# Performance work log

Measured on AMD Instinct MI355X. Metric: run time of the kernel, lower is better.

Reference implementation:

```python
import jax, jax.numpy as jnp
import numpy as np
import math

EPS = 1e-5

def layernorm(x, g, b):
    mu = jnp.mean(x, axis=-1, keepdims=True)
    var = jnp.var(x, axis=-1, keepdims=True)
    return (x - mu) * jax.lax.rsqrt(var + EPS) * g + b

def setup_inputs() -> dict:
    key = jax.random.key(0)
    ks = jax.random.split(key, 12)
    B, T, E, H = 4, 2048, 128, 8
    D = H * E          # 1024
    F = 4 * D          # 4096
    s = 0.02
    return {
        "X":     jax.random.normal(ks[0], (B, T, E), jnp.float32),
        "ln1_g": jnp.ones((E,), jnp.float32),
        "ln1_b": jnp.zeros((E,), jnp.float32),
        "Wq":    jax.random.normal(ks[1], (H, E, E), jnp.float32) * s,
        "bq":    jax.random.normal(ks[2], (H, E), jnp.float32) * s,
        "Wk":    jax.random.normal(ks[3], (H, E, E), jnp.float32) * s,
        "bk":    jax.random.normal(ks[4], (H, E), jnp.float32) * s,
        "Wv":    jax.random.normal(ks[5], (H, E, E), jnp.float32) * s,
        "bv":    jax.random.normal(ks[6], (H, E), jnp.float32) * s,
        "ln2_g": jnp.ones((D,), jnp.float32),
        "ln2_b": jnp.zeros((D,), jnp.float32),
        "W1":    jax.random.normal(ks[7], (D, F), jnp.float32) * s,
        "b1":    jax.random.normal(ks[8], (F,), jnp.float32) * s,
        "W2":    jax.random.normal(ks[9], (F, E), jnp.float32) * s,
        "b2":    jax.random.normal(ks[10], (E,), jnp.float32) * s,
    }

def reference(X, ln1_g, ln1_b, Wq, bq, Wk, bk, Wv, bv, ln2_g, ln2_b, W1, b1, W2, b2):
    B, T, E = X.shape
    Xn = layernorm(X, ln1_g, ln1_b)                       # [B,T,E]
    # per-head projections, vectorized over heads
    q = jnp.einsum('bte,hef->bhtf', Xn, Wq) + bq[None, :, None, :]
    k = jnp.einsum('bte,hef->bhtf', Xn, Wk) + bk[None, :, None, :]
    v = jnp.einsum('bte,hef->bhtf', Xn, Wv) + bv[None, :, None, :]
    scores = jnp.einsum('bhtf,bhsf->bhts', q, k) / math.sqrt(E)
    # causal mask: positions with s > t set to -inf (triu offset=1)
    t_idx = jnp.arange(T)
    mask = t_idx[None, :] > t_idx[:, None]                # [T,S], True above diag
    scores = jnp.where(mask[None, None], -jnp.inf, scores)
    # NOTE: original code softmaxes over dim = ndim-2, i.e. the QUERY axis
    attn = jax.nn.softmax(scores, axis=-2)
    out = jnp.einsum('bhts,bhsf->bhtf', attn, v)          # [B,H,T,E]
    # concat heads along last dim (head order preserved)
    concat = jnp.transpose(out, (0, 2, 1, 3)).reshape(B, T, -1)  # [B,T,H*E]
    h = layernorm(concat, ln2_g, ln2_b)
    mid = jax.nn.gelu(h @ W1 + b1, approximate=False)
    return mid @ W2 + b2                                   # [B,T,E]
```

## Files before the change

### kernel.cpp

```cpp
#include <hip/hip_runtime.h>
#include <hip/hip_bf16.h>
#include <math.h>

typedef __hip_bfloat16 bf16;
typedef __attribute__((ext_vector_type(8))) short short8;
typedef __attribute__((ext_vector_type(4))) float floatx4;

#define B_ 4
#define T_ 2048
#define E_ 128
#define H_ 8
#define D_ 1024
#define F_ 4096
#define M_ 8192

static __device__ __forceinline__ float b2f(bf16 v){ return __bfloat162float(v); }
static __device__ __forceinline__ bf16  f2b(float v){ return __float2bfloat16(v); }
static __device__ __forceinline__ short f2bs(float v){ bf16 h = __float2bfloat16(v); return *(short*)&h; }

static __device__ __forceinline__ void glds16(const bf16* g, void* l){
  __builtin_amdgcn_global_load_lds((const __attribute__((address_space(1))) void*)g,
                                   (__attribute__((address_space(3))) void*)l, 16, 0, 0);
}

__global__ void detect_dtype_k(const unsigned int* __restrict__ g, int* __restrict__ flag){
  if (threadIdx.x == 0) flag[0] = (g[0] == 0x3F803F80u) ? 1 : 0;
}

__global__ void convert_misc_k(const void* s0, const void* s1, const void* s2, const void* s3,
                               const void* s4, const void* s5, const void* s6, const void* s7,
                               const void* s8,
                               bf16* g1, bf16* b1, bf16* bqkv, bf16* g2, bf16* b2l,
                               bf16* bb1, bf16* bb2, const int* __restrict__ flag){
  int i = blockIdx.x * 256 + threadIdx.x;
  if (i >= 9600) return;
  int fl = flag[0];
  const void* src; bf16* dst; int off;
  if      (i <  128){ src = s0; dst = g1;          off = i;        }
  else if (i <  256){ src = s1; dst = b1;          off = i - 128;  }
  else if (i < 1280){ src = s2; dst = bqkv;        off = i - 256;  }
  else if (i < 2304){ src = s3; dst = bqkv + 1024; off = i - 1280; }
  else if (i < 3328){ src = s4; dst = bqkv + 2048; off = i - 2304; }
  else if (i < 4352){ src = s5; dst = g2;          off = i - 3328; }
  else if (i < 5376){ src = s6; dst = b2l;         off = i - 4352; }
  else if (i < 9472){ src = s7; dst = bb1;         off = i - 5376; }
  else              { src = s8; dst = bb2;         off = i - 9472; }
  dst[off] = fl ? ((const bf16*)src)[off] : f2b(((const float*)src)[off]);
}

__global__ __launch_bounds__(256) void transpose_cvt_k(const void* __restrict__ src, bf16* __restrict__ dst,
                                                       int R, int C, const int* __restrict__ flag){
  __shared__ float tile[32][33];
  int r0 = blockIdx.y * 32, c0 = blockIdx.x * 32;
  int tx = threadIdx.x & 31, ty = threadIdx.x >> 5;
  int fl = flag[0];
  #pragma unroll
  for (int i = 0; i < 32; i += 8){
    size_t idx = (size_t)(r0 + ty + i) * C + c0 + tx;
    tile[ty + i][tx] = fl ? b2f(((const bf16*)src)[idx]) : ((const float*)src)[idx];
  }
  __syncthreads();
  #pragma unroll
  for (int i = 0; i < 32; i += 8){
    dst[(size_t)(c0 + ty + i) * R + r0 + tx] = f2b(tile[tx][ty + i]);
  }
}

__global__ __launch_bounds__(256) void transpose_qkv_k(const void* __restrict__ Wq, const void* __restrict__ Wk,
                                                       const void* __restrict__ Wv, bf16* __restrict__ dst,
                                                       const int* __restrict__ flag){
  __shared__ float tile[32][33];
  int sel = blockIdx.z >> 3, h = blockIdx.z & 7;
  const void* src = (sel == 0) ? Wq : (sel == 1) ? Wk : Wv;
  size_t mo = (size_t)h * E_ * E_;
  bf16* d = dst + (size_t)sel * H_ * E_ * E_ + mo;
  int r0 = blockIdx.y * 32, c0 = blockIdx.x * 32;
  int tx = threadIdx.x & 31, ty = threadIdx.x >> 5;
  int fl = flag[0];
  #pragma unroll
  for (int i = 0; i < 32; i += 8){
    size_t idx = mo + (size_t)(r0 + ty + i) * E_ + c0 + tx;
    tile[ty + i][tx] = fl ? b2f(((const bf16*)src)[idx]) : ((const float*)src)[idx];
  }
  __syncthreads();
  #pragma unroll
  for (int i = 0; i < 32; i += 8){
    d[(size_t)(c0 + ty + i) * E_ + r0 + tx] = f2b(tile[tx][ty + i]);
  }
}

__global__ __launch_bounds__(256) void ln1_k(const void* __restrict__ X, const bf16* __restrict__ g,
                                             const bf16* __restrict__ b, bf16* __restrict__ out,
                                             const int* __restrict__ flag){
  int row = blockIdx.x * 4 + (threadIdx.x >> 6);
  int lane = threadIdx.x & 63;
  float x0, x1;
  if (flag[0]){
    const bf16* xp = (const bf16*)X + (size_t)row * E_;
    x0 = b2f(xp[lane]); x1 = b2f(xp[lane + 64]);
  } else {
    const float* xp = (const float*)X + (size_t)row * E_;
    x0 = xp[lane]; x1 = xp[lane + 64];
  }
  float s  = x0 + x1;
  float s2 = x0 * x0 + x1 * x1;
  #pragma unroll
  for (int o = 32; o > 0; o >>= 1){ s += __shfl_xor(s, o, 64); s2 += __shfl_xor(s2, o, 64); }
  float mu  = s * (1.0f / 128.0f);
  float var = s2 * (1.0f / 128.0f) - mu * mu;
  float rs  = rsqrtf(var + 1e-5f);
  out[(size_t)row * E_ + lane]      = f2b((x0 - mu) * rs * b2f(g[lane])      + b2f(b[lane]));
  out[(size_t)row * E_ + lane + 64] = f2b((x1 - mu) * rs * b2f(g[lane + 64]) + b2f(b[lane + 64]));
}

template<int EPI>
__global__ __launch_bounds__(256, 3) void gemm_mfma_k(
    const bf16* __restrict__ A, const bf16* __restrict__ Bt,
    const bf16* __restrict__ bias, void* __restrict__ out,
    int K, const int* __restrict__ flag)
{
  __shared__ __align__(16) short As[2][4][128][8];
  __shared__ __align__(16) short Bs[2][4][128][8];
  int tid = threadIdx.x;
  int lane = tid & 63, w = tid >> 6;
  int quad = lane >> 4, l16 = lane & 15;
  int wm = w & 1, wn = w >> 1;
  int m0 = blockIdx.y * 128;
  int n0, nit;
  size_t kstart;
  if (EPI == 3){ n0 = 0; int kc = K >> 3; kstart = (size_t)blockIdx.x * kc; nit = kc >> 5; }
  else         { n0 = blockIdx.x * 128; kstart = 0; nit = K >> 5; }

  int seg0 = w * 2, seg1 = w * 2 + 1;
  int kq0 = seg0 & 3, mb0 = (seg0 >> 2) * 64;
  int kq1 = seg1 & 3, mb1 = (seg1 >> 2) * 64;
  const bf16* pa0 = A  + (size_t)(m0 + mb0 + lane) * K + kstart + kq0 * 8;
  const bf16* pa1 = A  + (size_t)(m0 + mb1 + lane) * K + kstart + kq1 * 8;
  const bf16* pb0 = Bt + (size_t)(n0 + mb0 + lane) * K + kstart + kq0 * 8;
  const bf16* pb1 = Bt + (size_t)(n0 + mb1 + lane) * K + kstart + kq1 * 8;
  uint4 ra0 = *(const uint4*)pa0, ra1 = *(const uint4*)pa1;
  uint4 rb0 = *(const uint4*)pb0, rb1 = *(const uint4*)pb1;

  floatx4 acc[4][4];
  #pragma unroll
  for (int i = 0; i < 4; i++)
    #pragma unroll
    for (int j = 0; j < 4; j++) acc[i][j] = (floatx4){0.f, 0.f, 0.f, 0.f};

  for (int it = 0; it < nit; it++){
    int buf = it & 1;
    *(uint4*)&As[buf][kq0][mb0 + lane][0] = ra0;
    *(uint4*)&As[buf][kq1][mb1 + lane][0] = ra1;
    *(uint4*)&Bs[buf][kq0][mb0 + lane][0] = rb0;
    *(uint4*)&Bs[buf][kq1][mb1 + lane][0] = rb1;
    __syncthreads();
    if (it + 1 < nit){
      int ko = (it + 1) << 5;
      ra0 = *(const uint4*)(pa0 + ko); ra1 = *(const uint4*)(pa1 + ko);
      rb0 = *(const uint4*)(pb0 + ko); rb1 = *(const uint4*)(pb1 + ko);
    }
    short8 af[4], bfr[4];
    #pragma unroll
    for (int i = 0; i < 4; i++) af[i]  = *(const short8*)&As[buf][quad][wm * 64 + i * 16 + l16][0];
    #pragma unroll
    for (int j = 0; j < 4; j++) bfr[j] = *(const short8*)&Bs[buf][quad][wn * 64 + j * 16 + l16][0];
    #pragma unroll
    for (int i = 0; i < 4; i++)
      #pragma unroll
      for (int j = 0; j < 4; j++)
        acc[i][j] = __builtin_amdgcn_mfma_f32_16x16x32_bf16(af[i], bfr[j], acc[i][j], 0, 0, 0);
  }

  bf16* po = (EPI == 3) ? (bf16*)out + (size_t)blockIdx.x * M_ * E_ : nullptr;
  #pragma unroll
  for (int i = 0; i < 4; i++){
    #pragma unroll
    for (int j = 0; j < 4; j++){
      int nn = n0 + wn * 64 + j * 16 + l16;
      float bv = (EPI == 3) ? 0.0f : b2f(bias[nn]);
      if (EPI == 0){
        int sel = nn >> 10, h = (nn >> 7) & 7, f = nn & 127;
        size_t SZ = (size_t)B_ * H_ * T_ * E_;
        int mmb = m0 + wm * 64 + i * 16 + quad * 4;
        int b = mmb >> 11, t = mmb & (T_ - 1);
        if (sel < 2){
          #pragma unroll
          for (int r = 0; r < 4; r++)
            ((bf16*)out)[(size_t)sel * SZ + (((size_t)(b * H_ + h) * T_ + t + r) * E_) + f] =
              f2b(acc[i][j][r] + bv);
        } else {
          ushort4 pk;
          #pragma unroll
          for (int r = 0; r < 4; r++) ((short*)&pk)[r] = f2bs(acc[i][j][r] + bv);
          *(ushort4*)((bf16*)out + 2 * SZ + (((size_t)(b * H_ + h) * E_ + f) * T_) + t) = pk;
        }
      } else {
        #pragma unroll
        for (int r = 0; r < 4; r++){
          int mm = m0 + wm * 64 + i * 16 + quad * 4 + r;
          po[(size_t)mm * E_ + nn] = f2b(acc[i][j][r] + bv);
        }
      }
    }
  }
}

__global__ __launch_bounds__(512, 2) void mlp1_swz_k(
    const bf16* __restrict__ A, const bf16* __restrict__ Bt,
    const bf16* __restrict__ bias, bf16* __restrict__ out)
{
  __shared__ __align__(16) short As[4][256][32];
  __shared__ __align__(16) short Bs[4][256][32];
  constexpr int K  = D_;
  constexpr int NK = K / 32;
  constexpr int BUFB = 256 * 32 * 2;

  int tid = threadIdx.x;
  int lane = tid & 63, w = tid >> 6;
  int quad = lane >> 4, l16 = lane & 15;
  int wm = w & 1, wn = w >> 1;
  int orig = blockIdx.y * 16 + blockIdx.x;
  int swz = (orig & 7) * 64 + (orig >> 3);
  int m0 = (swz >> 4) * 256, n0 = (swz & 15) * 256;

  int u0 = w * 2, u1 = u0 + 1;
  int rl = lane >> 2;
  int cg = (lane & 3) ^ ((lane >> 3) & 3);
  const bf16* gA0 = A  + (size_t)(m0 + u0 * 16 + rl) * K + cg * 8;
  const bf16* gA1 = A  + (size_t)(m0 + u1 * 16 + rl) * K + cg * 8;
  const bf16* gB0 = Bt + (size_t)(n0 + u0 * 16 + rl) * K + cg * 8;
  const bf16* gB1 = Bt + (size_t)(n0 + u1 * 16 + rl) * K + cg * 8;

  int offA[2][4], offB[4];
  #pragma unroll
  for (int h = 0; h < 2; h++)
    #pragma unroll
    for (int i = 0; i < 4; i++){
      int ra = wm * 128 + h * 64 + i * 16 + l16;
      offA[h][i] = (ra << 6) + ((quad ^ ((ra >> 1) & 3)) << 4);
    }
  #pragma unroll
  for (int j = 0; j < 4; j++){
    int rb = wn * 64 + j * 16 + l16;
    offB[j] = (rb << 6) + ((quad ^ ((rb >> 1) & 3)) << 4);
  }

  #pragma unroll
  for (int t = 0; t < 3; t++){
    int ko = t * 32;
    glds16(gA0 + ko, &As[t][u0 * 16][0]);
    glds16(gA1 + ko, &As[t][u1 * 16][0]);
    glds16(gB0 + ko, &Bs[t][u0 * 16][0]);
    glds16(gB1 + ko, &Bs[t][u1 * 16][0]);
  }
  asm volatile("s_waitcnt vmcnt(8)" ::: "memory");
  __builtin_amdgcn_s_barrier();

  floatx4 acc[2][4][4];
  #pragma unroll
  for (int h = 0; h < 2; h++)
    #pragma unroll
    for (int i = 0; i < 4; i++)
      #pragma unroll
      for (int j = 0; j < 4; j++) acc[h][i][j] = (floatx4){0.f, 0.f, 0.f, 0.f};

  #pragma unroll 1
  for (int k = 0; k < NK; ++k){
    int bk = k & 3, b3 = (k + 3) & 3;
    const char* baseA = (const char*)As + bk * BUFB;
    const char* baseB = (const char*)Bs + bk * BUFB;
    short8 bf8[4], a2[2][4];
    #pragma unroll
    for (int j = 0; j < 4; j++) bf8[j]   = *(const short8*)(baseB + offB[j]);
    #pragma unroll
    for (int i = 0; i < 4; i++) a2[0][i] = *(const short8*)(baseA + offA[0][i]);
    #pragma unroll
    for (int i = 0; i < 4; i++) a2[1][i] = *(const short8*)(baseA + offA[1][i]);
    if (k + 3 < NK){
      int ko = (k + 3) * 32;
      glds16(gA0 + ko, &As[b3][u0 * 16][0]);
      glds16(gA1 + ko, &As[b3][u1 * 16][0]);
      glds16(gB0 + ko, &Bs[b3][u0 * 16][0]);
      glds16(gB1 + ko, &Bs[b3][u1 * 16][0]);
    }
    __builtin_amdgcn_s_setprio(1);
    #pragma unroll
    for (int h = 0; h < 2; h++)
      #pragma unroll
      for (int i = 0; i < 4; i++)
        #pragma unroll
        for (int j = 0; j < 4; j++)
          acc[h][i][j] = __builtin_amdgcn_mfma_f32_16x16x32_bf16(a2[h][i], bf8[j], acc[h][i][j], 0, 0, 0);
    __builtin_amdgcn_s_setprio(0);
    if (k < NK - 3)       { asm volatile("s_waitcnt vmcnt(8)" ::: "memory"); }
    else if (k == NK - 3) { asm volatile("s_waitcnt vmcnt(4)" ::: "memory"); }
    else if (k == NK - 2) { asm volatile("s_waitcnt vmcnt(0)" ::: "memory"); }
    asm volatile("s_waitcnt lgkmcnt(0)" ::: "memory");
    __builtin_amdgcn_sched_barrier(0);
    __builtin_amdgcn_s_barrier();
  }

  #pragma unroll
  for (int h = 0; h < 2; h++){
    #pragma unroll
    for (int i = 0; i < 4; i++){
      #pragma unroll
      for (int j = 0; j < 4; j++){
        int nn = n0 + wn * 64 + j * 16 + l16;
        float bv = b2f(bias[nn]);
        #pragma unroll
        for (int r = 0; r < 4; r++){
          int mm = m0 + wm * 128 + h * 64 + i * 16 + quad * 4 + r;
          float v = acc[h][i][j][r] + bv;
          float e = __expf(1.5957691216057308f * v * (1.0f + 0.044715f * v * v));
          out[(size_t)mm * F_ + nn] = f2b(v - v / (1.0f + e));
        }
      }
    }
  }
}

__global__ __launch_bounds__(256) void mlp2_fin_k(const bf16* __restrict__ P, const bf16* __restrict__ bias,
                                                  void* __restrict__ out, const int* __restrict__ flag){
  int i = blockIdx.x * 256 + threadIdx.x;
  const size_t S = (size_t)M_ * E_;
  float v = b2f(bias[i & (E_ - 1)]);
  #pragma unroll
  for (int k = 0; k < 8; k++) v += b2f(P[i + k * S]);
  if (flag[0]) ((bf16*)out)[i] = f2b(v);
  else         ((float*)out)[i] = v;
}

__global__ __launch_bounds__(256, 2) void colstats_k(const bf16* __restrict__ Q, const bf16* __restrict__ K,
                                                     float* __restrict__ IL){
  __shared__ __align__(16) short Qs[2][128][128];
  __shared__ float lcol[64];
  const float scale = 0.0883883476483184f;
  int tid = threadIdx.x;
  int lane = tid & 63, w = tid >> 6;
  int quad = lane >> 4, l16 = lane & 15;
  int x = blockIdx.x;
  int bh = x & 31, sblk = x >> 5;
  int s0 = sblk * 64;

  short8 bk[4][4];
  #pragma unroll
  for (int j = 0; j < 4; j++)
    #pragma unroll
    for (int kb = 0; kb < 4; kb++)
      bk[j][kb] = *(const short8*)(K + ((size_t)bh * T_ + s0 + j * 16 + l16) * E_ + kb * 32 + quad * 8);

  if (tid < 64) lcol[tid] = 0.0f;

  int t0s = (s0 / 128) * 128;
  int nit = (T_ - t0s) >> 7;

  int srow = lane >> 4, schunk = lane & 15;
  #pragma unroll
  for (int t2 = 0; t2 < 8; t2++){
    int u = w * 8 + t2;
    int r = u * 4 + srow;
    const bf16* ga = Q + ((size_t)bh * T_ + t0s + r) * E_ + (schunk ^ (r & 7)) * 8;
    glds16(ga, &Qs[0][u * 4][0]);
  }
  __syncthreads();

  float part[4] = {0.f, 0.f, 0.f, 0.f};
  for (int it = 0; it < nit; it++){
    int buf = it & 1;
    if (it + 1 < nit){
      int nb = buf ^ 1;
      int t1 = t0s + ((it + 1) << 7);
      #pragma unroll
      for (int t2 = 0; t2 < 8; t2++){
        int u = w * 8 + t2;
        int r = u * 4 + srow;
        const bf16* ga = Q + ((size_t)bh * T_ + t1 + r) * E_ + (schunk ^ (r & 7)) * 8;
        glds16(ga, &Qs[nb][u * 4][0]);
      }
    }
    floatx4 acc[2][4];
    #pragma unroll
    for (int i = 0; i < 2; i++)
      #pragma unroll
      for (int j = 0; j < 4; j++) acc[i][j] = (floatx4){0.f, 0.f, 0.f, 0.f};
    #pragma unroll
    for (int kb = 0; kb < 4; kb++){
      short8 af[2];
      #pragma unroll
      for (int i = 0; i < 2; i++){
        int row = w * 32 + i * 16 + l16;
        af[i] = *(const short8*)((const char*)&Qs[buf][0][0] + (row << 8)
                                 + ((((kb << 2) + quad) ^ (l16 & 7)) << 4));
      }
      #pragma unroll
      for (int i = 0; i < 2; i++)
        #pragma unroll
        for (int j = 0; j < 4; j++)
          acc[i][j] = __builtin_amdgcn_mfma_f32_16x16x32_bf16(af[i], bk[j][kb], acc[i][j], 0, 0, 0);
    }
    int t0 = t0s + (it << 7);
    bool dtile = (it == 0);
    #pragma unroll
    for (int i = 0; i < 2; i++)
      #pragma unroll
      for (int j = 0; j < 4; j++)
        #pragma unroll
        for (int r = 0; r < 4; r++){
          float e = __expf(acc[i][j][r] * scale);
          if (dtile){
            int t = t0 + w * 32 + i * 16 + quad * 4 + r;
            int s = s0 + j * 16 + l16;
            if (t < s) e = 0.0f;
          }
          part[j] += e;
        }
    __syncthreads();
  }
  #pragma unroll
  for (int j = 0; j < 4; j++){
    part[j] += __shfl_xor(part[j], 16, 64);
    part[j] += __shfl_xor(part[j], 32, 64);
  }
  if (quad == 0){
    #pragma unroll
    for (int j = 0; j < 4; j++) atomicAdd(&lcol[j * 16 + l16], part[j]);
  }
  __syncthreads();
  if (tid < 64) IL[(size_t)bh * T_ + s0 + tid] = 1.0f / lcol[tid];
}

__global__ __launch_bounds__(256, 2) void attnout_k(const bf16* __restrict__ Q, const bf16* __restrict__ K,
                                                    const bf16* __restrict__ VT, const float* __restrict__ IL,
                                                    bf16* __restrict__ CC){
  __shared__ __align__(16) short Ks[64][128];
  __shared__ __align__(16) short Vs[128][64];
  __shared__ __align__(16) short Ps[128][72];
  const float scale = 0.0883883476483184f;
  int tid = threadIdx.x;
  int lane = tid & 63, w = tid >> 6;
  int quad = lane >> 4, l16 = lane & 15;
  int x = blockIdx.x;
  int bh = x & 31, tblk = x >> 5;
  int t0 = tblk * 128;
  int b = bh >> 3, h = bh & 7;

  short8 qf[2][4];
  #pragma unroll
  for (int i = 0; i < 2; i++)
    #pragma unroll
    for (int kb = 0; kb < 4; kb++)
      qf[i][kb] = *(const short8*)(Q + ((size_t)bh * T_ + t0 + w * 32 + i * 16 + l16) * E_ + kb * 32 + quad * 8);

  floatx4 O[2][8];
  #pragma unroll
  for (int i = 0; i < 2; i++)
    #pragma unroll
    for (int n = 0; n < 8; n++) O[i][n] = (floatx4){0.f, 0.f, 0.f, 0.f};

  int ksrow = lane >> 4, kschunk = lane & 15;
  int vsrow = lane >> 3, vschunk = lane & 7;

  for (int s0 = 0; s0 < t0 + 128; s0 += 64){
    __syncthreads();
    #pragma unroll
    for (int t = 0; t < 4; t++){
      int u = w * 4 + t;
      int r = u * 4 + ksrow;
      const bf16* ga = K + ((size_t)bh * T_ + s0 + r) * E_ + ((kschunk ^ (r & 7)) * 8);
      glds16(ga, &Ks[u * 4][0]);
    }
    #pragma unroll
    for (int t = 0; t < 4; t++){
      int u = w * 4 + t;
      int e = u * 8 + vsrow;
      const bf16* ga = VT + ((size_t)bh * E_ + e) * T_ + s0 + ((vschunk ^ (e & 7)) * 8);
      glds16(ga, &Vs[u * 8][0]);
    }
    __syncthreads();
    floatx4 acc[2][4];
    #pragma unroll
    for (int i = 0; i < 2; i++)
      #pragma unroll
      for (int j = 0; j < 4; j++) acc[i][j] = (floatx4){0.f, 0.f, 0.f, 0.f};
    __builtin_amdgcn_s_setprio(1);
    #pragma unroll
    for (int kb = 0; kb < 4; kb++){
      short8 bfr[4];
      #pragma unroll
      for (int j = 0; j < 4; j++)
        bfr[j] = *(const short8*)&Ks[j * 16 + l16][(((kb << 2) + quad) ^ (l16 & 7)) * 8];
      #pragma unroll
      for (int i = 0; i < 2; i++)
        #pragma unroll
        for (int j = 0; j < 4; j++)
          acc[i][j] = __builtin_amdgcn_mfma_f32_16x16x32_bf16(qf[i][kb], bfr[j], acc[i][j], 0, 0, 0);
    }
    __builtin_amdgcn_s_setprio(0);
    float il[4];
    #pragma unroll
    for (int j = 0; j < 4; j++) il[j] = IL[(size_t)bh * T_ + s0 + j * 16 + l16];
    bool dtile = (s0 + 63 > t0);
    #pragma unroll
    for (int i = 0; i < 2; i++)
      #pragma unroll
      for (int j = 0; j < 4; j++)
        #pragma unroll
        for (int r = 0; r < 4; r++){
          float p = __expf(acc[i][j][r] * scale) * il[j];
          int trow = w * 32 + i * 16 + quad * 4 + r;
          if (dtile){
            int t = t0 + trow, s = s0 + j * 16 + l16;
            if (t < s) p = 0.0f;
          }
          Ps[trow][j * 16 + l16] = f2bs(p);
        }
    __syncthreads();
    __builtin_amdgcn_s_setprio(1);
    #pragma unroll
    for (int kb2 = 0; kb2 < 2; kb2++){
      short8 pa[2], vb[8];
      #pragma unroll
      for (int i = 0; i < 2; i++) pa[i] = *(const short8*)&Ps[w * 32 + i * 16 + l16][kb2 * 32 + quad * 8];
      #pragma unroll
      for (int n = 0; n < 8; n++)
        vb[n] = *(const short8*)&Vs[n * 16 + l16][(((kb2 << 2) + quad) ^ (l16 & 7)) * 8];
      #pragma unroll
      for (int i = 0; i < 2; i++)
        #pragma unroll
        for (int n = 0; n < 8; n++)
          O[i][n] = __builtin_amdgcn_mfma_f32_16x16x32_bf16(pa[i], vb[n], O[i][n], 0, 0, 0);
    }
    __builtin_amdgcn_s_setprio(0);
  }
  #pragma unroll
  for (int i = 0; i < 2; i++)
    #pragma unroll
    for (int n = 0; n < 8; n++)
      #pragma unroll
      for (int r = 0; r < 4; r++){
        int t = t0 + w * 32 + i * 16 + quad * 4 + r;
        int e = n * 16 + l16;
        CC[((size_t)(b * T_ + t)) * D_ + h * E_ + e] = f2b(O[i][n][r]);
      }
}

__global__ __launch_bounds__(256) void ln2_k(const bf16* __restrict__ in, const bf16* __restrict__ g,
                                             const bf16* __restrict__ bta, bf16* __restrict__ out){
  __shared__ float wsum[4], wsum2[4];
  int row = blockIdx.x, tid = threadIdx.x;
  const bf16* xp = in + (size_t)row * D_;
  float x[4]; float s = 0.0f, s2 = 0.0f;
  #pragma unroll
  for (int i = 0; i < 4; i++){ x[i] = b2f(xp[tid + i * 256]); s += x[i]; s2 += x[i] * x[i]; }
  #pragma unroll
  for (int o = 32; o > 0; o >>= 1){ s += __shfl_xor(s, o, 64); s2 += __shfl_xor(s2, o, 64); }
  int wid = tid >> 6;
  if ((tid & 63) == 0){ wsum[wid] = s; wsum2[wid] = s2; }
  __syncthreads();
  s  = wsum[0] + wsum[1] + wsum[2] + wsum[3];
  s2 = wsum2[0] + wsum2[1] + wsum2[2] + wsum2[3];
  float mu  = s * (1.0f / 1024.0f);
  float var = s2 * (1.0f / 1024.0f) - mu * mu;
  float rs  = rsqrtf(var + 1e-5f);
  #pragma unroll
  for (int i = 0; i < 4; i++){
    int c = tid + i * 256;
    out[(size_t)row * D_ + c] = f2b((x[i] - mu) * rs * b2f(g[c]) + b2f(bta[c]));
  }
}

static constexpr size_t A256(size_t x){ return (x + 255) & ~(size_t)255; }

extern "C" void kernel_launch(void* const* d_in, const int* in_sizes, int n_in,
                              void* d_out, int out_size, void* d_ws, size_t ws_size,
                              hipStream_t stream){
  (void)in_sizes; (void)n_in; (void)out_size; (void)ws_size;
  char* ws = (char*)d_ws;

  constexpr size_t o_flag  = 0;
  constexpr size_t o_g1    = 256;
  constexpr size_t o_b1    = A256(o_g1    + (size_t)E_ * 2);
  constexpr size_t o_WqkvT = A256(o_b1    + (size_t)E_ * 2);
  constexpr size_t o_bqkv  = A256(o_WqkvT + (size_t)3 * H_ * E_ * E_ * 2);
  constexpr size_t o_g2    = A256(o_bqkv  + (size_t)3 * H_ * E_ * 2);
  constexpr size_t o_b2l   = A256(o_g2    + (size_t)D_ * 2);
  constexpr size_t o_W1T   = A256(o_b2l   + (size_t)D_ * 2);
  constexpr size_t o_bb1   = A256(o_W1T   + (size_t)D_ * F_ * 2);
  constexpr size_t o_W2T   = A256(o_bb1   + (size_t)F_ * 2);
  constexpr size_t o_bb2   = A256(o_W2T   + (size_t)F_ * E_ * 2);
  constexpr size_t o_xn    = A256(o_bb2   + (size_t)E_ * 2);
  constexpr size_t o_q     = A256(o_xn    + (size_t)M_ * E_ * 2);
  constexpr size_t o_k     = o_q + (size_t)B_ * H_ * T_ * E_ * 2;
  constexpr size_t o_vt    = o_k + (size_t)B_ * H_ * T_ * E_ * 2;
  constexpr size_t o_il    = A256(o_vt + (size_t)B_ * H_ * T_ * E_ * 2);
  constexpr size_t o_cc    = A256(o_il + (size_t)B_ * H_ * T_ * 4);
  constexpr size_t o_h2    = A256(o_cc + (size_t)M_ * D_ * 2);
  constexpr size_t o_mid   = o_q;
  constexpr size_t o_part  = o_h2;
  static_assert(o_mid + (size_t)M_ * F_ * 2 <= o_h2, "mid overlaps live h2 buffer");
  static_assert((size_t)8 * M_ * E_ * 2 <= (size_t)M_ * D_ * 2, "partials exceed h2 region");

  int*  flag  = (int*)(ws + o_flag);
  bf16* g1    = (bf16*)(ws + o_g1);
  bf16* b1p   = (bf16*)(ws + o_b1);
  bf16* WqkvT = (bf16*)(ws + o_WqkvT);
  bf16* bqkv  = (bf16*)(ws + o_bqkv);
  bf16* g2    = (bf16*)(ws + o_g2);
  bf16* b2l   = (bf16*)(ws + o_b2l);
  bf16* W1T   = (bf16*)(ws + o_W1T);
  bf16* bb1   = (bf16*)(ws + o_bb1);
  bf16* W2T   = (bf16*)(ws + o_W2T);
  bf16* bb2   = (bf16*)(ws + o_bb2);
  bf16* xn    = (bf16*)(ws + o_xn);
  bf16* Qb    = (bf16*)(ws + o_q);
  bf16* Kb    = (bf16*)(ws + o_k);
  bf16* VTb   = (bf16*)(ws + o_vt);
  float* ILp  = (float*)(ws + o_il);
  bf16* ccp   = (bf16*)(ws + o_cc);
  bf16* h2p   = (bf16*)(ws + o_h2);
  bf16* midp  = (bf16*)(ws + o_mid);
  bf16* part  = (bf16*)(ws + o_part);

  detect_dtype_k<<<1, 64, 0, stream>>>((const unsigned int*)d_in[1], flag);

  convert_misc_k<<<38, 256, 0, stream>>>(d_in[1], d_in[2], d_in[4], d_in[6], d_in[8],
                                         d_in[9], d_in[10], d_in[12], d_in[14],
                                         g1, b1p, bqkv, g2, b2l, bb1, bb2, flag);

  transpose_qkv_k<<<dim3(4, 4, 24), 256, 0, stream>>>(d_in[3], d_in[5], d_in[7], WqkvT, flag);
  transpose_cvt_k<<<dim3(F_ / 32, D_ / 32), 256, 0, stream>>>(d_in[11], W1T, D_, F_, flag);
  transpose_cvt_k<<<dim3(E_ / 32, F_ / 32), 256, 0, stream>>>(d_in[13], W2T, F_, E_, flag);

  ln1_k<<<M_ / 4, 256, 0, stream>>>(d_in[0], g1, b1p, xn, flag);

  gemm_mfma_k<0><<<dim3(3 * D_ / 128, M_ / 128), 256, 0, stream>>>(xn, WqkvT, bqkv, Qb, E_, flag);

  colstats_k<<<1024, 256, 0, stream>>>(Qb, Kb, ILp);
  attnout_k<<<512, 256, 0, stream>>>(Qb, Kb, VTb, ILp, ccp);

  ln2_k<<<M_, 256, 0, stream>>>(ccp, g2, b2l, h2p);

  mlp1_swz_k<<<dim3(F_ / 256, M_ / 256), 512, 0, stream>>>(h2p, W1T, bb1, midp);
  gemm_mfma_k<3><<<dim3(8, M_ / 128), 256, 0, stream>>>(midp, W2T, bb2, part, F_, flag);
  mlp2_fin_k<<<M_ * E_ / 256, 256, 0, stream>>>(part, bb2, d_out, flag);
}
```

Baseline: 351.4 us.

## Use direct global-to-LDS coalesced loads with XOR-swizzled layout in small GEMMs

```diff
diff --git a/kernel.cpp b/kernel.cpp
--- a/kernel.cpp
+++ b/kernel.cpp
@@ -114,13 +114,13 @@
 }
 
 template<int EPI>
-__global__ __launch_bounds__(256, 3) void gemm_mfma_k(
+__global__ __launch_bounds__(256, 3) void gemm_coal_k(
     const bf16* __restrict__ A, const bf16* __restrict__ Bt,
     const bf16* __restrict__ bias, void* __restrict__ out,
     int K, const int* __restrict__ flag)
 {
-  __shared__ __align__(16) short As[2][4][128][8];
-  __shared__ __align__(16) short Bs[2][4][128][8];
+  __shared__ __align__(16) short As[2][128][32];
+  __shared__ __align__(16) short Bs[2][128][32];
   int tid = threadIdx.x;
   int lane = tid & 63, w = tid >> 6;
   int quad = lane >> 4, l16 = lane & 15;
@@ -131,15 +131,29 @@
   if (EPI == 3){ n0 = 0; int kc = K >> 3; kstart = (size_t)blockIdx.x * kc; nit = kc >> 5; }
   else         { n0 = blockIdx.x * 128; kstart = 0; nit = K >> 5; }
 
-  int seg0 = w * 2, seg1 = w * 2 + 1;
-  int kq0 = seg0 & 3, mb0 = (seg0 >> 2) * 64;
-  int kq1 = seg1 & 3, mb1 = (seg1 >> 2) * 64;
-  const bf16* pa0 = A  + (size_t)(m0 + mb0 + lane) * K + kstart + kq0 * 8;
-  const bf16* pa1 = A  + (size_t)(m0 + mb1 + lane) * K + kstart + kq1 * 8;
-  const bf16* pb0 = Bt + (size_t)(n0 + mb0 + lane) * K + kstart + kq0 * 8;
-  const bf16* pb1 = Bt + (size_t)(n0 + mb1 + lane) * K + kstart + kq1 * 8;
-  uint4 ra0 = *(const uint4*)pa0, ra1 = *(const uint4*)pa1;
-  uint4 rb0 = *(const uint4*)pb0, rb1 = *(const uint4*)pb1;
+  int rl = lane >> 2;
+  int cg = (lane & 3) ^ ((lane >> 3) & 3);
+  int u0 = w * 2, u1 = u0 + 1;
+  const bf16* gA0 = A  + (size_t)(m0 + u0 * 16 + rl) * K + kstart + cg * 8;
+  const bf16* gA1 = A  + (size_t)(m0 + u1 * 16 + rl) * K + kstart + cg * 8;
+  const bf16* gB0 = Bt + (size_t)(n0 + u0 * 16 + rl) * K + kstart + cg * 8;
+  const bf16* gB1 = Bt + (size_t)(n0 + u1 * 16 + rl) * K + kstart + cg * 8;
+
+  int offA[4], offB[4];
+  #pragma unroll
+  for (int i = 0; i < 4; i++){
+    int ra = wm * 64 + i * 16 + l16;
+    offA[i] = (ra << 6) + ((quad ^ ((ra >> 1) & 3)) << 4);
+    int rb = wn * 64 + i * 16 + l16;
+    offB[i] = (rb << 6) + ((quad ^ ((rb >> 1) & 3)) << 4);
+  }
+
+  glds16(gA0, &As[0][u0 * 16][0]);
+  glds16(gA1, &As[0][u1 * 16][0]);
+  glds16(gB0, &Bs[0][u0 * 16][0]);
+  glds16(gB1, &Bs[0][u1 * 16][0]);
+  asm volatile("s_waitcnt vmcnt(0)" ::: "memory");
+  __builtin_amdgcn_s_barrier();
 
   floatx4 acc[4][4];
   #pragma unroll
@@ -147,28 +161,34 @@
     #pragma unroll
     for (int j = 0; j < 4; j++) acc[i][j] = (floatx4){0.f, 0.f, 0.f, 0.f};
 
+  #pragma unroll 1
   for (int it = 0; it < nit; it++){
     int buf = it & 1;
-    *(uint4*)&As[buf][kq0][mb0 + lane][0] = ra0;
-    *(uint4*)&As[buf][kq1][mb1 + lane][0] = ra1;
-    *(uint4*)&Bs[buf][kq0][mb0 + lane][0] = rb0;
-    *(uint4*)&Bs[buf][kq1][mb1 + lane][0] = rb1;
-    __syncthreads();
     if (it + 1 < nit){
       int ko = (it + 1) << 5;
-      ra0 = *(const uint4*)(pa0 + ko); ra1 = *(const uint4*)(pa1 + ko);
-      rb0 = *(const uint4*)(pb0 + ko); rb1 = *(const uint4*)(pb1 + ko);
-    }
+      glds16(gA0 + ko, &As[buf ^ 1][u0 * 16][0]);
+      glds16(gA1 + ko, &As[buf ^ 1][u1 * 16][0]);
+      glds16(gB0 + ko, &Bs[buf ^ 1][u0 * 16][0]);
+      glds16(gB1 + ko, &Bs[buf ^ 1][u1 * 16][0]);
+    }
+    const char* bA = (const char*)&As[buf][0][0];
+    const char* bB = (const char*)&Bs[buf][0][0];
     short8 af[4], bfr[4];
     #pragma unroll
-    for (int i = 0; i < 4; i++) af[i]  = *(const short8*)&As[buf][quad][wm * 64 + i * 16 + l16][0];
-    #pragma unroll
-    for (int j = 0; j < 4; j++) bfr[j] = *(const short8*)&Bs[buf][quad][wn * 64 + j * 16 + l16][0];
+    for (int i = 0; i < 4; i++) af[i]  = *(const short8*)(bA + offA[i]);
+    #pragma unroll
+    for (int j = 0; j < 4; j++) bfr[j] = *(const short8*)(bB + offB[j]);
+    __builtin_amdgcn_s_setprio(1);
     #pragma unroll
     for (int i = 0; i < 4; i++)
       #pragma unroll
       for (int j = 0; j < 4; j++)
         acc[i][j] = __builtin_amdgcn_mfma_f32_16x16x32_bf16(af[i], bfr[j], acc[i][j], 0, 0, 0);
+    __builtin_amdgcn_s_setprio(0);
+    if (it + 1 < nit){ asm volatile("s_waitcnt vmcnt(0)" ::: "memory"); }
+    asm volatile("s_waitcnt lgkmcnt(0)" ::: "memory");
+    __builtin_amdgcn_sched_barrier(0);
+    __builtin_amdgcn_s_barrier();
   }
 
   bf16* po = (EPI == 3) ? (bf16*)out + (size_t)blockIdx.x * M_ * E_ : nullptr;
@@ -634,7 +654,7 @@
 
   ln1_k<<<M_ / 4, 256, 0, stream>>>(d_in[0], g1, b1p, xn, flag);
 
-  gemm_mfma_k<0><<<dim3(3 * D_ / 128, M_ / 128), 256, 0, stream>>>(xn, WqkvT, bqkv, Qb, E_, flag);
+  gemm_coal_k<0><<<dim3(3 * D_ / 128, M_ / 128), 256, 0, stream>>>(xn, WqkvT, bqkv, Qb, E_, flag);
 
   colstats_k<<<1024, 256, 0, stream>>>(Qb, Kb, ILp);
   attnout_k<<<512, 256, 0, stream>>>(Qb, Kb, VTb, ILp, ccp);
@@ -642,6 +662,6 @@
   ln2_k<<<M_, 256, 0, stream>>>(ccp, g2, b2l, h2p);
 
   mlp1_swz_k<<<dim3(F_ / 256, M_ / 256), 512, 0, stream>>>(h2p, W1T, bb1, midp);
-  gemm_mfma_k<3><<<dim3(8, M_ / 128), 256, 0, stream>>>(midp, W2T, bb2, part, F_, flag);
+  gemm_coal_k<3><<<dim3(8, M_ / 128), 256, 0, stream>>>(midp, W2T, bb2, part, F_, flag);
   mlp2_fin_k<<<M_ * E_ / 256, 256, 0, stream>>>(part, bb2, d_out, flag);
 }
```

After: 346.1 us. No clear change (-1.5%).
